# Optimization experiments

Hardware: AMD Instinct MI355X
Metric: run time of the kernel (lower is better)

The kernel has to match this reference:

```python
import jax, jax.numpy as jnp
import numpy as np

B, N, D = 4, 4096, 1024
H, DH = 16, 64  # heads, dim_head; inner_dim = H*DH = 1024
EPS = 1e-6


def setup_inputs() -> dict:
    key = jax.random.key(0)
    ks = jax.random.split(key, 6)
    s = 1.0 / np.sqrt(D)
    return {
        "x": jax.random.normal(ks[0], (B, N, D), dtype=jnp.float32),
        "Wq": jax.random.normal(ks[1], (D, H * DH), dtype=jnp.float32) * s,
        "Wk": jax.random.normal(ks[2], (D, H * DH), dtype=jnp.float32) * s,
        "Wv": jax.random.normal(ks[3], (D, H * DH), dtype=jnp.float32) * s,
        "Wo": jax.random.normal(ks[4], (H * DH, D), dtype=jnp.float32) * s,
        "bo": jnp.zeros((D,), dtype=jnp.float32),
    }


def reference(x, Wq, Wk, Wv, Wo, bo):
    # projections, split heads: b n (h d) -> b h n d
    def split_heads(t):
        b, n, _ = t.shape
        return t.reshape(b, n, H, DH).transpose(0, 2, 1, 3)

    q = split_heads(x @ Wq)
    k = split_heads(x @ Wk)  # context = x (self-attention)
    v = split_heads(x @ Wv)

    # elu feature map: elu(x) + 1
    q = jax.nn.elu(q) + 1.0
    k = jax.nn.elu(k) + 1.0

    # normalizer z[b,h,n,1] = q . sum_n k  + eps
    k_sum = k.sum(axis=2)                                  # b h d
    z = jnp.einsum('bhnd,bhd->bhn', q, k_sum)[..., None] + EPS

    # kv outer-product reduction: O(N d^2)
    kv = jnp.einsum('bhnd,bhne->bhde', k, v)               # b h d e
    out = jnp.einsum('bhnd,bhde->bhne', q, kv) / z         # b h n e

    # merge heads: b h n d -> b n (h d)
    out = out.transpose(0, 2, 1, 3).reshape(x.shape[0], x.shape[1], H * DH)
    return out @ Wo + bo
```

## Files before the change

### kernel.cpp

```cpp
#include <hip/hip_runtime.h>
#include <hip/hip_bf16.h>


#define DEV_INLINE __device__ __forceinline__

typedef short bf16x8 __attribute__((ext_vector_type(8)));
typedef float f32x4  __attribute__((ext_vector_type(4)));

static constexpr int Bb = 4, Nn = 4096, Dd = 1024, Hh = 16, DHd = 64;
static constexpr int Mrows = Bb * Nn;

DEV_INLINE float bf2f(short s) {
  unsigned u = ((unsigned)(unsigned short)s) << 16;
  float f; __builtin_memcpy(&f, &u, 4); return f;
}
DEV_INLINE short f2bf(float f) {
  unsigned u; __builtin_memcpy(&u, &f, 4);
  unsigned r = (u + 0x7fffu + ((u >> 16) & 1u)) >> 16;
  return (short)r;
}

DEV_INLINE void gload16(const void* g, void* l) {
  typedef __attribute__((address_space(1))) const void gv_t;
  typedef __attribute__((address_space(3))) void lv_t;
  __builtin_amdgcn_global_load_lds((gv_t*)g, (lv_t*)l, 16, 0, 0);
}

DEV_INLINE int lds_off(int r_, int c_) {
  return r_ * 128 + ((((c_ >> 3) ^ (r_ & 7)) << 3) | (c_ & 7));
}

__global__ void prep_kernel(const float* __restrict__ x,
                            const float* __restrict__ Wq, const float* __restrict__ Wk,
                            const float* __restrict__ Wv, const float* __restrict__ Wo,
                            short* __restrict__ xb, short* __restrict__ Wt,
                            short* __restrict__ WoT, float* __restrict__ ksum) {
  int z = blockIdx.z;
  int t = threadIdx.x;
  if (z == 4) {
    int bid = blockIdx.y * 64 + blockIdx.x;
    const int total = Mrows * 1024 / 4;
    for (int i = bid * 256 + t; i < total; i += 1024 * 256) {
      float4 v = ((const float4*)x)[i];
      short4 o;
      o.x = f2bf(v.x); o.y = f2bf(v.y); o.z = f2bf(v.z); o.w = f2bf(v.w);
      ((short4*)xb)[i] = o;
    }
    return;
  }
  if (blockIdx.x >= 16) return;
  if (z == 0 && blockIdx.y == 0)
    ksum[blockIdx.x * 256 + t] = 0.f;
  const float* W = (z == 0) ? Wq : (z == 1) ? Wk : (z == 2) ? Wv : Wo;
  short* dstb = (z < 3) ? (Wt + (size_t)z * 1024 * 1024) : WoT;
  __shared__ float tile[64][69];
  int r = t >> 2, c4 = (t & 3) << 4;
  const float* src = W + (blockIdx.y * 64 + r) * 1024 + blockIdx.x * 64 + c4;
  for (int j = 0; j < 4; ++j) {
    float4 v = ((const float4*)src)[j];
    tile[r][c4 + 4 * j + 0] = v.x;
    tile[r][c4 + 4 * j + 1] = v.y;
    tile[r][c4 + 4 * j + 2] = v.z;
    tile[r][c4 + 4 * j + 3] = v.w;
  }
  __syncthreads();
  __attribute__((aligned(16))) short tmp[16];
  for (int j = 0; j < 16; ++j) tmp[j] = f2bf(tile[c4 + j][r]);
  short* dst = dstb + (blockIdx.x * 64 + r) * 1024 + blockIdx.y * 64 + c4;
  ((int4*)dst)[0] = ((int4*)tmp)[0];
  ((int4*)dst)[1] = ((int4*)tmp)[1];
}

template <int MODE>
__global__ __launch_bounds__(256, 4) void gemm128_kernel(
    const short* __restrict__ A, const short* __restrict__ Bt,
    short* __restrict__ q, short* __restrict__ kT, short* __restrict__ vT,
    float* __restrict__ out, const float* __restrict__ bias,
    float* __restrict__ ksum, int nTilesN) {
  __shared__ __align__(16) short sm[128 * 128];
  short* smA = sm;
  short* smB = sm + 8192;
  const int K = 1024;
  int bid0 = blockIdx.x;
  int xcd = bid0 & 7, local = bid0 >> 3;
  int chunk = local >> 6, rem = local & 63;
  int ncc = nTilesN >> 3;
  int cm = chunk / ncc, cn = chunk % ncc;
  int tm = xcd * 16 + cm * 8 + (rem >> 3);
  int tn = cn * 8 + (rem & 7);

  int t = threadIdx.x, w = t >> 6, lane = t & 63;
  int rl = lane & 15, kg = lane >> 4;
  int wr = w >> 1, wc = w & 1;
  const short* Abase = A + (size_t)tm * 128 * K;
  const short* Bbase = Bt + (size_t)tn * 128 * K;

  f32x4 acc[4][4] = {};
  for (int k0 = 0; k0 < K; k0 += 64) {
    __syncthreads();
    for (int p = 0; p < 4; ++p) {
      int c = p * 256 + t;
      int row = c >> 3, u = c & 7;
      int off = ((u ^ (row & 7)) << 3);
      gload16(Abase + row * K + k0 + off, (char*)smA + p * 4096 + w * 1024);
      gload16(Bbase + row * K + k0 + off, (char*)smB + p * 4096 + w * 1024);
    }
    __syncthreads();
    for (int kk = 0; kk < 2; ++kk) {
      int slot = kk * 4 + kg;
      bf16x8 af[4], bfr[4];
      for (int mt = 0; mt < 4; ++mt) {
        int row = wr * 64 + mt * 16 + rl;
        af[mt] = *(const bf16x8*)&smA[row * 64 + ((slot ^ (row & 7)) << 3)];
      }
      for (int nt = 0; nt < 4; ++nt) {
        int row = wc * 64 + nt * 16 + rl;
        bfr[nt] = *(const bf16x8*)&smB[row * 64 + ((slot ^ (row & 7)) << 3)];
      }
      for (int mt = 0; mt < 4; ++mt)
        for (int nt = 0; nt < 4; ++nt)
          acc[mt][nt] = __builtin_amdgcn_mfma_f32_16x16x32_bf16(af[mt], bfr[nt], acc[mt][nt], 0, 0, 0);
    }
  }
  if (MODE == 1) {
    float* smf = (float*)sm;
    __syncthreads();
    for (int h = 0; h < 2; ++h) {
      if (wr == h) {
        for (int mt = 0; mt < 4; ++mt)
          for (int nt = 0; nt < 4; ++nt)
            for (int r = 0; r < 4; ++r)
              smf[(mt * 16 + kg * 4 + r) * 128 + wc * 64 + nt * 16 + rl] = acc[mt][nt][r];
      }
      __syncthreads();
      for (int i = 0; i < 8; ++i) {
        int idx = i * 256 + t;
        int row = idx >> 5, c4 = (idx & 31) << 2;
        float4 v = *(const float4*)&smf[row * 128 + c4];
        float4 bv = *(const float4*)&bias[tn * 128 + c4];
        v.x += bv.x; v.y += bv.y; v.z += bv.z; v.w += bv.w;
        *(float4*)&out[(size_t)(tm * 128 + h * 64 + row) * Dd + tn * 128 + c4] = v;
      }
      __syncthreads();
    }
    return;
  }
  __syncthreads();
  int sec = tn >> 3;
  int tloc = tn & 7;
  for (int mt = 0; mt < 4; ++mt)
    for (int nt = 0; nt < 4; ++nt)
      for (int r = 0; r < 4; ++r) {
        float v = acc[mt][nt][r];
        if (sec <= 1) v = v > 0.f ? v + 1.f : __expf(v);
        int row = wr * 64 + mt * 16 + kg * 4 + r;
        int col = wc * 64 + nt * 16 + rl;
        int o = (sec == 0) ? lds_off(row, col) : lds_off(col, row);
        sm[o] = f2bf(v);
      }
  __syncthreads();
  if (sec == 0) {
    for (int i = 0; i < 8; ++i) {
      int idx = i * 256 + t;
      int row = idx >> 4, c = idx & 15;
      int col0 = c * 8;
      int gcol = tloc * 128 + col0;
      int h = gcol >> 6, d0 = gcol & 63;
      int grow = tm * 128 + row;
      int b = grow >> 12, n = grow & 4095;
      *(int4*)&q[(((size_t)(b * Hh + h)) * Nn + n) * DHd + d0] = *(const int4*)&sm[lds_off(row, col0)];
    }
  } else {
    short* dst = (sec == 1) ? kT : vT;
    for (int i = 0; i < 8; ++i) {
      int idx = i * 256 + t;
      int dcol = idx >> 4, c = idx & 15;
      int n0 = c * 8;
      int gcol = tloc * 128 + dcol;
      int h = gcol >> 6, d = gcol & 63;
      int grow0 = tm * 128 + n0;
      int b = grow0 >> 12, n = grow0 & 4095;
      *(int4*)&dst[(((size_t)(b * Hh + h)) * DHd + d) * Nn + n] = *(const int4*)&sm[lds_off(dcol, n0)];
    }
    if (sec == 1) {
      int dcol = t >> 1, half = t & 1;
      float s = 0.f;
      for (int c = half * 64; c < half * 64 + 64; ++c)
        s += bf2f(sm[lds_off(dcol, c)]);
      s += __shfl_xor(s, 1);
      if (half == 0) {
        int g = tloc * 128 + dcol;
        int h = g >> 6, d = g & 63;
        int b = (tm * 128) >> 12;
        atomicAdd(&ksum[(b * Hh + h) * DHd + d], s);
      }
    }
  }
}

__global__ __launch_bounds__(256, 2) void kv_kernel(const short* __restrict__ kT,
                                                    const short* __restrict__ vT,
                                                    float* __restrict__ kvp) {
  int lid = blockIdx.x;
  int xcd = lid & 7, j = lid >> 3;
  int b = xcd >> 1;
  int seg = (xcd & 1) * 4 + (j & 3);
  int h = j >> 2;
  int bh = b * 16 + h;
  __shared__ __align__(16) short smK[64 * 128];
  __shared__ __align__(16) short smV[64 * 128];
  int t = threadIdx.x;
  int w = t >> 6, lane = t & 63, rl = lane & 15, kg = lane >> 4;
  const short* kb = kT + (size_t)bh * DHd * Nn + seg * 512;
  const short* vb = vT + (size_t)bh * DHd * Nn + seg * 512;
  f32x4 acc[4] = {};
  for (int n0 = 0; n0 < 512; n0 += 128) {
    __syncthreads();
    for (int p = 0; p < 4; ++p) {
      int c = p * 256 + t;
      int row = c >> 4, u = c & 15;
      int off = ((u ^ (row & 15)) << 3);
      gload16(kb + row * Nn + n0 + off, (char*)smK + p * 4096 + w * 1024);
      gload16(vb + row * Nn + n0 + off, (char*)smV + p * 4096 + w * 1024);
    }
    __syncthreads();
    for (int kk = 0; kk < 4; ++kk) {
      int slot = kk * 4 + kg;
      int rowA = w * 16 + rl;
      bf16x8 av = *(const bf16x8*)&smK[rowA * 128 + ((slot ^ (rowA & 15)) << 3)];
      for (int nt = 0; nt < 4; ++nt) {
        int rowB = nt * 16 + rl;
        bf16x8 bv = *(const bf16x8*)&smV[rowB * 128 + ((slot ^ (rowB & 15)) << 3)];
        acc[nt] = __builtin_amdgcn_mfma_f32_16x16x32_bf16(av, bv, acc[nt], 0, 0, 0);
      }
    }
  }
  float* smf = (float*)smK;
  __syncthreads();
  for (int nt = 0; nt < 4; ++nt)
    for (int r = 0; r < 4; ++r)
      smf[(nt * 16 + rl) * 64 + (w * 16 + kg * 4 + r)] = acc[nt][r];
  __syncthreads();
  float* dst = kvp + ((size_t)(bh * 8 + seg)) * 4096;
  for (int i = 0; i < 4; ++i) {
    int idx = i * 256 + t;
    int e = idx >> 4, c4 = (idx & 15) << 2;
    *(float4*)&dst[e * 64 + c4] = *(const float4*)&smf[e * 64 + c4];
  }
}

__global__ void kvc_kernel(const float* __restrict__ kvp, short* __restrict__ kvT) {
  int bh = blockIdx.x, t = threadIdx.x;
  const float* p0 = kvp + (size_t)bh * 8 * 4096;
  for (int rep = 0; rep < 4; ++rep) {
    int idx = rep * 1024 + t * 4;
    float4 s = *(const float4*)&p0[idx];
    for (int j = 1; j < 8; ++j) {
      float4 aa = *(const float4*)&p0[j * 4096 + idx];
      s.x += aa.x; s.y += aa.y; s.z += aa.z; s.w += aa.w;
    }
    short4 o;
    o.x = f2bf(s.x); o.y = f2bf(s.y); o.z = f2bf(s.z); o.w = f2bf(s.w);
    *(short4*)&kvT[(size_t)bh * 4096 + idx] = o;
  }
}

__global__ __launch_bounds__(256, 2) void attn_kernel(const short* __restrict__ q,
                                                      const short* __restrict__ kvT,
                                                      const float* __restrict__ ksum,
                                                      short* __restrict__ attn) {
  int lid = blockIdx.x;
  int xcd = lid & 7, j = lid >> 3;
  int b = xcd >> 1;
  int rb = (xcd & 1) * 32 + (j & 31);
  int h = j >> 5;
  int bh = b * 16 + h;
  __shared__ float sks[64];
  __shared__ __align__(16) short satt[64 * 64];
  int t = threadIdx.x, w = t >> 6, lane = t & 63, rl = lane & 15, kg = lane >> 4;
  if (t < 64) sks[t] = ksum[bh * 64 + t];
  __syncthreads();
  int row0 = rb * 64 + w * 16;
  const short* qb = q + ((size_t)bh * Nn + row0) * DHd;
  const short* kvb = kvT + (size_t)bh * 4096;
  f32x4 acc[4] = {};
  float zp = 0.f;
  for (int kk = 0; kk < 2; ++kk) {
    int kb = kk * 32 + kg * 8;
    bf16x8 av = *(const bf16x8*)&qb[rl * DHd + kb];
    for (int jj = 0; jj < 8; ++jj) zp += bf2f(av[jj]) * sks[kb + jj];
    for (int nt = 0; nt < 4; ++nt) {
      bf16x8 bfr = *(const bf16x8*)&kvb[(nt * 16 + rl) * 64 + kb];
      acc[nt] = __builtin_amdgcn_mfma_f32_16x16x32_bf16(av, bfr, acc[nt], 0, 0, 0);
    }
  }
  zp += __shfl_xor(zp, 16);
  zp += __shfl_xor(zp, 32);
  float zr[4];
  for (int r = 0; r < 4; ++r) zr[r] = __shfl(zp, kg * 4 + r);
  for (int nt = 0; nt < 4; ++nt)
    for (int r = 0; r < 4; ++r)
      satt[(w * 16 + kg * 4 + r) * 64 + nt * 16 + rl] = f2bf(acc[nt][r] / (zr[r] + 1e-6f));
  __syncthreads();
  for (int i = 0; i < 2; ++i) {
    int idx = i * 256 + t;
    int row = idx >> 3, c8 = (idx & 7) << 3;
    int n = rb * 64 + row;
    *(int4*)&attn[((size_t)(b * Nn + n)) * 1024 + h * 64 + c8] = *(const int4*)&satt[row * 64 + c8];
  }
}

extern "C" void kernel_launch(void* const* d_in, const int* in_sizes, int n_in,
                              void* d_out, int out_size, void* d_ws, size_t ws_size,
                              hipStream_t stream) {
  const float* x  = (const float*)d_in[0];
  const float* Wq = (const float*)d_in[1];
  const float* Wk = (const float*)d_in[2];
  const float* Wv = (const float*)d_in[3];
  const float* Wo = (const float*)d_in[4];
  const float* bo = (const float*)d_in[5];
  float* out = (float*)d_out;

  char* ws = (char*)d_ws;
  size_t off = 0;
  auto alloc = [&](size_t bytes) {
    char* p = ws + off;
    off += (bytes + 255) & ~(size_t)255;
    return p;
  };
  short* xb   = (short*)alloc((size_t)Mrows * 1024 * 2);
  short* Wt   = (short*)alloc((size_t)3072 * 1024 * 2);
  short* WoT  = (short*)alloc((size_t)1024 * 1024 * 2);
  short* qb   = (short*)alloc((size_t)64 * Nn * DHd * 2);
  short* kT   = (short*)alloc((size_t)64 * DHd * Nn * 2);
  short* vT   = (short*)alloc((size_t)64 * DHd * Nn * 2);
  float* ksum = (float*)alloc((size_t)64 * 64 * 4);
  float* kvp  = (float*)alloc((size_t)64 * 8 * 4096 * 4);
  short* kvT  = (short*)alloc((size_t)64 * 4096 * 2);
  short* attn = (short*)alloc((size_t)Mrows * 1024 * 2);

  prep_kernel<<<dim3(64, 16, 5), 256, 0, stream>>>(x, Wq, Wk, Wv, Wo, xb, Wt, WoT, ksum);

  gemm128_kernel<0><<<3072, 256, 0, stream>>>(xb, Wt, qb, kT, vT, nullptr, nullptr, ksum, 24);
  kv_kernel<<<512, 256, 0, stream>>>(kT, vT, kvp);
  kvc_kernel<<<64, 256, 0, stream>>>(kvp, kvT);
  attn_kernel<<<4096, 256, 0, stream>>>(qb, kvT, ksum, attn);
  gemm128_kernel<1><<<1024, 256, 0, stream>>>(attn, WoT, nullptr, nullptr, nullptr, out, bo, nullptr, 8);
}
```

Baseline: 238.1 us.

## Fold kv partial reduction into atomics and bf16 conversion into attn kernel

Removes the separate kvc reduction kernel. kv_kernel blocks now atomically add their fp32 partial kv tiles into a single buffer that prep_kernel zeroes, and attn_kernel converts that fp32 kv to bf16 into swizzled LDS itself. Grid mappings drop the XCD-aware block remapping and attn occupancy is raised to 4 blocks per CU. This saves one launch and the partial-buffer traffic, but adds float atomics, redundant per-block kv conversion across 4096 blocks, and nondeterministic summation order.

Result: slower. 254.1 us (+6.7%).

```diff
diff --git a/kernel.cpp b/kernel.cpp
--- a/kernel.cpp
+++ b/kernel.cpp
@@ -34,7 +34,8 @@
                             const float* __restrict__ Wq, const float* __restrict__ Wk,
                             const float* __restrict__ Wv, const float* __restrict__ Wo,
                             short* __restrict__ xb, short* __restrict__ Wt,
-                            short* __restrict__ WoT, float* __restrict__ ksum) {
+                            short* __restrict__ WoT, float* __restrict__ ksum,
+                            float* __restrict__ kvf) {
   int z = blockIdx.z;
   int t = threadIdx.x;
   if (z == 4) {
@@ -51,6 +52,11 @@
   if (blockIdx.x >= 16) return;
   if (z == 0 && blockIdx.y == 0)
     ksum[blockIdx.x * 256 + t] = 0.f;
+  if (z == 1 && blockIdx.y == 0) {
+    float4* p = (float4*)kvf;
+    int base = (blockIdx.x * 256 + t) * 16;
+    for (int j = 0; j < 16; ++j) p[base + j] = make_float4(0.f, 0.f, 0.f, 0.f);
+  }
   const float* W = (z == 0) ? Wq : (z == 1) ? Wk : (z == 2) ? Wv : Wo;
   short* dstb = (z < 3) ? (Wt + (size_t)z * 1024 * 1024) : WoT;
   __shared__ float tile[64][69];
@@ -200,15 +206,10 @@
 
 __global__ __launch_bounds__(256, 2) void kv_kernel(const short* __restrict__ kT,
                                                     const short* __restrict__ vT,
-                                                    float* __restrict__ kvp) {
-  int lid = blockIdx.x;
-  int xcd = lid & 7, j = lid >> 3;
-  int b = xcd >> 1;
-  int seg = (xcd & 1) * 4 + (j & 3);
-  int h = j >> 2;
-  int bh = b * 16 + h;
+                                                    float* __restrict__ kvf) {
   __shared__ __align__(16) short smK[64 * 128];
   __shared__ __align__(16) short smV[64 * 128];
+  int bh = blockIdx.x, seg = blockIdx.y;
   int t = threadIdx.x;
   int w = t >> 6, lane = t & 63, rl = lane & 15, kg = lane >> 4;
   const short* kb = kT + (size_t)bh * DHd * Nn + seg * 512;
@@ -241,56 +242,51 @@
     for (int r = 0; r < 4; ++r)
       smf[(nt * 16 + rl) * 64 + (w * 16 + kg * 4 + r)] = acc[nt][r];
   __syncthreads();
-  float* dst = kvp + ((size_t)(bh * 8 + seg)) * 4096;
+  float* dst = kvf + (size_t)bh * 4096;
   for (int i = 0; i < 4; ++i) {
-    int idx = i * 256 + t;
-    int e = idx >> 4, c4 = (idx & 15) << 2;
-    *(float4*)&dst[e * 64 + c4] = *(const float4*)&smf[e * 64 + c4];
-  }
-}
-
-__global__ void kvc_kernel(const float* __restrict__ kvp, short* __restrict__ kvT) {
-  int bh = blockIdx.x, t = threadIdx.x;
-  const float* p0 = kvp + (size_t)bh * 8 * 4096;
-  for (int rep = 0; rep < 4; ++rep) {
-    int idx = rep * 1024 + t * 4;
-    float4 s = *(const float4*)&p0[idx];
-    for (int j = 1; j < 8; ++j) {
-      float4 aa = *(const float4*)&p0[j * 4096 + idx];
-      s.x += aa.x; s.y += aa.y; s.z += aa.z; s.w += aa.w;
-    }
-    short4 o;
-    o.x = f2bf(s.x); o.y = f2bf(s.y); o.z = f2bf(s.z); o.w = f2bf(s.w);
-    *(short4*)&kvT[(size_t)bh * 4096 + idx] = o;
-  }
-}
-
-__global__ __launch_bounds__(256, 2) void attn_kernel(const short* __restrict__ q,
-                                                      const short* __restrict__ kvT,
+    int idx = i * 1024 + t * 4;
+    atomicAdd(&dst[idx + 0], smf[idx + 0]);
+    atomicAdd(&dst[idx + 1], smf[idx + 1]);
+    atomicAdd(&dst[idx + 2], smf[idx + 2]);
+    atomicAdd(&dst[idx + 3], smf[idx + 3]);
+  }
+}
+
+__global__ __launch_bounds__(256, 4) void attn_kernel(const short* __restrict__ q,
+                                                      const float* __restrict__ kvf,
                                                       const float* __restrict__ ksum,
                                                       short* __restrict__ attn) {
-  int lid = blockIdx.x;
-  int xcd = lid & 7, j = lid >> 3;
-  int b = xcd >> 1;
-  int rb = (xcd & 1) * 32 + (j & 31);
-  int h = j >> 5;
-  int bh = b * 16 + h;
+  int rb = blockIdx.x, bh = blockIdx.y;
+  int b = bh >> 4, h = bh & 15;
   __shared__ float sks[64];
+  __shared__ __align__(16) short skv[64 * 64];
   __shared__ __align__(16) short satt[64 * 64];
   int t = threadIdx.x, w = t >> 6, lane = t & 63, rl = lane & 15, kg = lane >> 4;
   if (t < 64) sks[t] = ksum[bh * 64 + t];
+  {
+    const float* kvb = kvf + (size_t)bh * 4096;
+    for (int i = 0; i < 4; ++i) {
+      int idx = i * 1024 + t * 4;
+      float4 v = *(const float4*)&kvb[idx];
+      int e = idx >> 6, c = idx & 63;
+      short4 o;
+      o.x = f2bf(v.x); o.y = f2bf(v.y); o.z = f2bf(v.z); o.w = f2bf(v.w);
+      *(short4*)&skv[e * 64 + (((c >> 3) ^ (e & 7)) << 3) + (c & 7)] = o;
+    }
+  }
   __syncthreads();
   int row0 = rb * 64 + w * 16;
   const short* qb = q + ((size_t)bh * Nn + row0) * DHd;
-  const short* kvb = kvT + (size_t)bh * 4096;
   f32x4 acc[4] = {};
   float zp = 0.f;
   for (int kk = 0; kk < 2; ++kk) {
     int kb = kk * 32 + kg * 8;
+    int slot = kk * 4 + kg;
     bf16x8 av = *(const bf16x8*)&qb[rl * DHd + kb];
     for (int jj = 0; jj < 8; ++jj) zp += bf2f(av[jj]) * sks[kb + jj];
     for (int nt = 0; nt < 4; ++nt) {
-      bf16x8 bfr = *(const bf16x8*)&kvb[(nt * 16 + rl) * 64 + kb];
+      int row = nt * 16 + rl;
+      bf16x8 bfr = *(const bf16x8*)&skv[row * 64 + ((slot ^ (row & 7)) << 3)];
       acc[nt] = __builtin_amdgcn_mfma_f32_16x16x32_bf16(av, bfr, acc[nt], 0, 0, 0);
     }
   }
@@ -335,15 +331,13 @@
   short* kT   = (short*)alloc((size_t)64 * DHd * Nn * 2);
   short* vT   = (short*)alloc((size_t)64 * DHd * Nn * 2);
   float* ksum = (float*)alloc((size_t)64 * 64 * 4);
-  float* kvp  = (float*)alloc((size_t)64 * 8 * 4096 * 4);
-  short* kvT  = (short*)alloc((size_t)64 * 4096 * 2);
+  float* kvf  = (float*)alloc((size_t)64 * 4096 * 4);
   short* attn = (short*)alloc((size_t)Mrows * 1024 * 2);
 
-  prep_kernel<<<dim3(64, 16, 5), 256, 0, stream>>>(x, Wq, Wk, Wv, Wo, xb, Wt, WoT, ksum);
+  prep_kernel<<<dim3(64, 16, 5), 256, 0, stream>>>(x, Wq, Wk, Wv, Wo, xb, Wt, WoT, ksum, kvf);
 
   gemm128_kernel<0><<<3072, 256, 0, stream>>>(xb, Wt, qb, kT, vT, nullptr, nullptr, ksum, 24);
-  kv_kernel<<<512, 256, 0, stream>>>(kT, vT, kvp);
-  kvc_kernel<<<64, 256, 0, stream>>>(kvp, kvT);
-  attn_kernel<<<4096, 256, 0, stream>>>(qb, kvT, ksum, attn);
+  kv_kernel<<<dim3(64, 8), 256, 0, stream>>>(kT, vT, kvf);
+  attn_kernel<<<dim3(64, 64), 256, 0, stream>>>(qb, kvf, ksum, attn);
   gemm128_kernel<1><<<1024, 256, 0, stream>>>(attn, WoT, nullptr, nullptr, nullptr, out, bo, nullptr, 8);
 }
```
